# Optimization experiments

Hardware: AMD Instinct MI355X
Metric: run time of the kernel (lower is better)

## Reference

```python
import jax, jax.numpy as jnp
import numpy as np

N_NODES = 100000
N_EDGES = 1600000
IN_FEATS = 128
OUT_FEATS = 64


def setup_inputs() -> dict:
    key = jax.random.key(0)
    k1, k2, k3, k4 = jax.random.split(key, 4)
    feat = jax.random.normal(k1, (N_NODES, IN_FEATS), dtype=jnp.float32)
    W = jax.random.normal(k2, (IN_FEATS, OUT_FEATS), dtype=jnp.float32) * (1.0 / np.sqrt(IN_FEATS))
    src = jax.random.randint(k3, (N_EDGES,), 0, N_NODES, dtype=jnp.int64)
    dst = jax.random.randint(k4, (N_EDGES,), 0, N_NODES, dtype=jnp.int64)
    return {"feat": feat, "W": W, "src": src, "dst": dst}


def reference(feat, W, src, dst):
    # Linear projection (bias=False): homogeneous graph -> shared fc
    ft = feat @ W  # [N, out]

    # per-edge dot-product score: e_ij = <ft[src], ft[dst]>
    a = jnp.sum(ft[src] * ft[dst], axis=-1)  # [E]

    # edge softmax segmented by destination node (numerically stable)
    neg_inf = jnp.finfo(a.dtype).min
    m = jax.ops.segment_max(a, dst, num_segments=N_NODES)  # [N]
    m = jnp.where(m == neg_inf, 0.0, m)  # guard zero-in-degree nodes
    e = jnp.exp(a - m[dst])  # [E]
    s = jax.ops.segment_sum(e, dst, num_segments=N_NODES)  # [N]
    s = jnp.where(s == 0.0, 1.0, s)
    sa = e / s[dst]  # [E]

    # weighted scatter-sum aggregation: out[i] = sum_{j in N(i)} sa_ij * ft[j]
    rst = jax.ops.segment_sum(ft[src] * sa[:, None], dst, num_segments=N_NODES)
    return rst
```

## Files before the change

kernel.cpp:

```cpp
#include <hip/hip_runtime.h>
#include <hip/hip_fp16.h>
#include <math.h>

#define N_NODES 100000
#define N_EDGES 1600000
#define IN_F    128
#define OUT_F   64
#define K_BKT     196
#define BKT_SHIFT 9
#define BKT_NODES 512
#define BKT_CAP   10240
#define CHUNK     4096
#define PBLKS     ((N_EDGES + CHUNK - 1) / CHUNK)
#define LTILES    (N_NODES / 16)
#define LBLKS     ((LTILES + 3) / 4)

typedef _Float16 half8 __attribute__((ext_vector_type(8)));
typedef float    f32x4 __attribute__((ext_vector_type(4)));


__global__ __launch_bounds__(256) void prep_kernel(const float* __restrict__ W,
                                                   _Float16* __restrict__ WT,
                                                   int* __restrict__ bcursor) {
    int t = threadIdx.x;
    if (t < K_BKT) bcursor[t] = 0;
    int n = t & 63, kh = t >> 6;
    _Float16 tmp[32];
#pragma unroll
    for (int j = 0; j < 32; ++j)
        tmp[j] = (_Float16)W[(size_t)(kh * 32 + j) * OUT_F + n];
#pragma unroll
    for (int v = 0; v < 4; ++v)
        *(half8*)(WT + (size_t)n * IN_F + kh * 32 + v * 8) = *(half8*)&tmp[v * 8];
}

__global__ __launch_bounds__(256) void partition_linear_kernel(const int* __restrict__ src,
                                                               const int* __restrict__ dst,
                                                               int* __restrict__ bcursor,
                                                               unsigned* __restrict__ staging,
                                                               const float* __restrict__ feat,
                                                               const _Float16* __restrict__ WT,
                                                               __half* __restrict__ fth) {
    __shared__ int hist[256], lbase[256], gbase[256], sc[256];
    __shared__ unsigned sval[CHUNK];
    __shared__ int spos[CHUNK];
    int t = threadIdx.x;
    if (blockIdx.x < PBLKS) {
        hist[t] = 0;
        __syncthreads();
        int beg = blockIdx.x * CHUNK;
        int end = min(beg + CHUNK, N_EDGES);
        for (int i = beg + t; i < end; i += 256)
            atomicAdd(&hist[dst[i] >> BKT_SHIFT], 1);
        __syncthreads();
        int v = hist[t];
        sc[t] = v;
        __syncthreads();
        for (int off = 1; off < 256; off <<= 1) {
            int add = (t >= off) ? sc[t - off] : 0;
            __syncthreads();
            sc[t] += add;
            __syncthreads();
        }
        lbase[t] = sc[t] - v;
        if (t < K_BKT && v) gbase[t] = t * BKT_CAP + atomicAdd(&bcursor[t], v);
        hist[t] = 0;
        __syncthreads();
        for (int i = beg + t; i < end; i += 256) {
            int s = src[i], d = dst[i];
            int b = d >> BKT_SHIFT;
            int r = atomicAdd(&hist[b], 1);
            int lp = lbase[b] + r;
            sval[lp] = (unsigned)s | ((unsigned)(d & (BKT_NODES - 1)) << 17);
            spos[lp] = gbase[b] + r;
        }
        __syncthreads();
        int n = end - beg;
        for (int p = t; p < n; p += 256) staging[spos[p]] = sval[p];
        return;
    }
    int gwave = (blockIdx.x - PBLKS) * 4 + (t >> 6);
    if (gwave >= LTILES) return;
    int lane = t & 63;
    int m = lane & 15, kg = lane >> 4;
    int r0 = gwave * 16;

    half8 fb[4][4];
#pragma unroll
    for (int kb = 0; kb < 4; ++kb)
#pragma unroll
        for (int nb = 0; nb < 4; ++nb)
            fb[kb][nb] = *(const half8*)(WT + (size_t)(nb * 16 + m) * IN_F + kb * 32 + kg * 8);

    f32x4 acc[4];
#pragma unroll
    for (int nb = 0; nb < 4; ++nb) acc[nb] = (f32x4){0.f, 0.f, 0.f, 0.f};

#pragma unroll
    for (int kb = 0; kb < 4; ++kb) {
        const float4* ap = (const float4*)(feat + (size_t)(r0 + m) * IN_F + kb * 32 + kg * 8);
        float4 a0 = ap[0], a1 = ap[1];
        half8 fa = {(_Float16)a0.x, (_Float16)a0.y, (_Float16)a0.z, (_Float16)a0.w,
                    (_Float16)a1.x, (_Float16)a1.y, (_Float16)a1.z, (_Float16)a1.w};
#pragma unroll
        for (int nb = 0; nb < 4; ++nb)
            acc[nb] = __builtin_amdgcn_mfma_f32_16x16x32_f16(fa, fb[kb][nb], acc[nb], 0, 0, 0);
    }
#pragma unroll
    for (int nb = 0; nb < 4; ++nb)
#pragma unroll
        for (int i = 0; i < 4; ++i)
            fth[(size_t)(r0 + kg * 4 + i) * OUT_F + nb * 16 + m] = __float2half_rn(acc[nb][i]);
}

__global__ __launch_bounds__(256) void place_kernel(const unsigned* __restrict__ staging,
                                                    const int* __restrict__ bcursor,
                                                    int* __restrict__ row_beg,
                                                    int* __restrict__ row_end,
                                                    int* __restrict__ edge_src) {
    __shared__ int cnt[BKT_NODES], sc[256], lcur[BKT_NODES];
    int t = threadIdx.x;
    cnt[t] = 0; cnt[t + 256] = 0;
    __syncthreads();
    int base = blockIdx.x * BKT_CAP;
    int n = bcursor[blockIdx.x];
    for (int i = t; i < n; i += 256)
        atomicAdd(&cnt[staging[base + i] >> 17], 1);
    __syncthreads();
    int v0 = cnt[2 * t], v1 = cnt[2 * t + 1];
    int ts = v0 + v1;
    sc[t] = ts;
    __syncthreads();
    for (int off = 1; off < 256; off <<= 1) {
        int add = (t >= off) ? sc[t - off] : 0;
        __syncthreads();
        sc[t] += add;
        __syncthreads();
    }
    int excl = sc[t] - ts;
    int node0 = blockIdx.x * BKT_NODES;
    int b0 = base + excl, b1 = base + excl + v0;
    lcur[2 * t]     = b0;
    lcur[2 * t + 1] = b1;
    if (node0 + 2 * t < N_NODES)     { row_beg[node0 + 2 * t] = b0;     row_end[node0 + 2 * t] = b0 + v0; }
    if (node0 + 2 * t + 1 < N_NODES) { row_beg[node0 + 2 * t + 1] = b1; row_end[node0 + 2 * t + 1] = b1 + v1; }
    __syncthreads();
    for (int i = base + t; i < base + n; i += 256) {
        unsigned u = staging[i];
        int pos = atomicAdd(&lcur[u >> 17], 1);
        edge_src[pos] = (int)(u & 0x1FFFFu);
    }
}

__global__ __launch_bounds__(256) void fused_node_kernel(const __half* __restrict__ fth,
                                                         const int* __restrict__ row_beg,
                                                         const int* __restrict__ row_end,
                                                         const int* __restrict__ edge_src,
                                                         float* __restrict__ out) {
    const float LOG2E = 1.44269504088896340736f;
    int wave = (blockIdx.x * 256 + threadIdx.x) >> 6;
    int lane = threadIdx.x & 63;
    if (wave >= N_NODES) return;
    int q = lane >> 4, ql = lane & 15;

    int beg = row_beg[wave];
    int end = row_end[wave];

    float2 rd = *(const float2*)(fth + (size_t)wave * OUT_F + 4 * ql);
    __half2 d01 = *(__half2*)&rd.x, d23 = *(__half2*)&rd.y;
    float fd0 = __half2float(d01.x) * LOG2E, fd1 = __half2float(d01.y) * LOG2E;
    float fd2 = __half2float(d23.x) * LOG2E, fd3 = __half2float(d23.y) * LOG2E;

    float m = -1e30f, l = 0.f;
    float a0 = 0.f, a1 = 0.f, a2 = 0.f, a3 = 0.f;

    for (int i = beg; i < end; i += 16) {
        int e0 = i + q, e1 = e0 + 4, e2 = e0 + 8, e3 = e0 + 12;
        bool u0 = e0 < end, u1 = e1 < end, u2 = e2 < end, u3 = e3 < end;
        int s0 = edge_src[u0 ? e0 : beg];
        int s1 = edge_src[u1 ? e1 : beg];
        int s2 = edge_src[u2 ? e2 : beg];
        int s3 = edge_src[u3 ? e3 : beg];
        float2 r0 = *(const float2*)(fth + (size_t)s0 * OUT_F + 4 * ql);
        float2 r1 = *(const float2*)(fth + (size_t)s1 * OUT_F + 4 * ql);
        float2 r2 = *(const float2*)(fth + (size_t)s2 * OUT_F + 4 * ql);
        float2 r3 = *(const float2*)(fth + (size_t)s3 * OUT_F + 4 * ql);
        __half2 A01 = *(__half2*)&r0.x, A23 = *(__half2*)&r0.y;
        __half2 B01 = *(__half2*)&r1.x, B23 = *(__half2*)&r1.y;
        __half2 C01 = *(__half2*)&r2.x, C23 = *(__half2*)&r2.y;
        __half2 D01 = *(__half2*)&r3.x, D23 = *(__half2*)&r3.y;
        float vA0 = __half2float(A01.x), vA1 = __half2float(A01.y);
        float vA2 = __half2float(A23.x), vA3 = __half2float(A23.y);
        float vB0 = __half2float(B01.x), vB1 = __half2float(B01.y);
        float vB2 = __half2float(B23.x), vB3 = __half2float(B23.y);
        float vC0 = __half2float(C01.x), vC1 = __half2float(C01.y);
        float vC2 = __half2float(C23.x), vC3 = __half2float(C23.y);
        float vD0 = __half2float(D01.x), vD1 = __half2float(D01.y);
        float vD2 = __half2float(D23.x), vD3 = __half2float(D23.y);

        float p0 = vA0 * fd0 + vA1 * fd1 + vA2 * fd2 + vA3 * fd3;
        float p1 = vB0 * fd0 + vB1 * fd1 + vB2 * fd2 + vB3 * fd3;
        float p2 = vC0 * fd0 + vC1 * fd1 + vC2 * fd2 + vC3 * fd3;
        float p3 = vD0 * fd0 + vD1 * fd1 + vD2 * fd2 + vD3 * fd3;
#pragma unroll
        for (int dd = 1; dd < 16; dd <<= 1) {
            p0 += __shfl_xor(p0, dd);
            p1 += __shfl_xor(p1, dd);
            p2 += __shfl_xor(p2, dd);
            p3 += __shfl_xor(p3, dd);
        }
        if (!u0) p0 = -1e30f;
        if (!u1) p1 = -1e30f;
        if (!u2) p2 = -1e30f;
        if (!u3) p3 = -1e30f;
        float nm = fmaxf(fmaxf(fmaxf(p0, p1), fmaxf(p2, p3)), m);
        float alpha = exp2f(m - nm);
        float w0 = exp2f(p0 - nm), w1 = exp2f(p1 - nm);
        float w2 = exp2f(p2 - nm), w3 = exp2f(p3 - nm);
        l = l * alpha + ((w0 + w1) + (w2 + w3));
        a0 = a0 * alpha + (w0 * vA0 + w1 * vB0) + (w2 * vC0 + w3 * vD0);
        a1 = a1 * alpha + (w0 * vA1 + w1 * vB1) + (w2 * vC1 + w3 * vD1);
        a2 = a2 * alpha + (w0 * vA2 + w1 * vB2) + (w2 * vC2 + w3 * vD2);
        a3 = a3 * alpha + (w0 * vA3 + w1 * vB3) + (w2 * vC3 + w3 * vD3);
        m = nm;
    }

#pragma unroll
    for (int dd = 16; dd <= 32; dd <<= 1) {
        float m2 = __shfl_xor(m, dd), l2 = __shfl_xor(l, dd);
        float b0 = __shfl_xor(a0, dd), b1 = __shfl_xor(a1, dd);
        float b2 = __shfl_xor(a2, dd), b3 = __shfl_xor(a3, dd);
        float M = fmaxf(m, m2);
        float e1 = exp2f(m - M), e2 = exp2f(m2 - M);
        l = l * e1 + l2 * e2;
        a0 = a0 * e1 + b0 * e2;
        a1 = a1 * e1 + b1 * e2;
        a2 = a2 * e1 + b2 * e2;
        a3 = a3 * e1 + b3 * e2;
        m = M;
    }
    if (q == 0) {
        float inv = (l > 0.f) ? 1.f / l : 0.f;
        *(float4*)(out + (size_t)wave * OUT_F + 4 * ql) =
            make_float4(a0 * inv, a1 * inv, a2 * inv, a3 * inv);
    }
}

extern "C" void kernel_launch(void* const* d_in, const int* in_sizes, int n_in,
                              void* d_out, int out_size, void* d_ws, size_t ws_size,
                              hipStream_t stream) {
    const float* feat = (const float*)d_in[0];
    const float* W    = (const float*)d_in[1];
    const int*   src  = (const int*)d_in[2];
    const int*   dst  = (const int*)d_in[3];
    float* out = (float*)d_out;

    __half*   fth      = (__half*)d_ws;
    unsigned* staging  = (unsigned*)((int*)d_ws + (size_t)N_NODES * OUT_F / 2);
    int*      edge_src = (int*)(staging + (size_t)K_BKT * BKT_CAP);
    int*      bcursor  = edge_src + (size_t)K_BKT * BKT_CAP;
    int*      row_beg  = bcursor + K_BKT;
    int*      row_end  = row_beg + N_NODES;
    _Float16* WT       = (_Float16*)(row_end + N_NODES);

    prep_kernel<<<1, 256, 0, stream>>>(W, WT, bcursor);
    partition_linear_kernel<<<PBLKS + LBLKS, 256, 0, stream>>>(src, dst, bcursor, staging,
                                                               feat, WT, fth);
    place_kernel<<<K_BKT, 256, 0, stream>>>(staging, bcursor, row_beg, row_end, edge_src);
    fused_node_kernel<<<(N_NODES * 64) / 256, 256, 0, stream>>>(fth, row_beg, row_end, edge_src, out);
}
```

Baseline: 205.0 us.

## Regroup pipeline stages and use 1024-thread blocks for partition and place

The prep kernel is dropped. The bucket-cursor reset becomes a memset, and the W transpose moves into an extra block of the partition kernel. The linear projection moves out of the partition launch and now runs alongside the bucket place step in a combined kernel. Partition and place now use 1024-thread blocks. The goal is fewer launches, better balance of the linear GEMM against the lighter place work, and more parallelism per bucket, at the cost of lower occupancy and more idle threads during the scans.

```diff
diff --git a/kernel.cpp b/kernel.cpp
--- a/kernel.cpp
+++ b/kernel.cpp
@@ -13,73 +13,112 @@
 #define CHUNK     4096
 #define PBLKS     ((N_EDGES + CHUNK - 1) / CHUNK)
 #define LTILES    (N_NODES / 16)
-#define LBLKS     ((LTILES + 3) / 4)
+#define LIN_BLKS  ((LTILES + 15) / 16)
 
 typedef _Float16 half8 __attribute__((ext_vector_type(8)));
 typedef float    f32x4 __attribute__((ext_vector_type(4)));
 
 
-__global__ __launch_bounds__(256) void prep_kernel(const float* __restrict__ W,
-                                                   _Float16* __restrict__ WT,
-                                                   int* __restrict__ bcursor) {
-    int t = threadIdx.x;
-    if (t < K_BKT) bcursor[t] = 0;
-    int n = t & 63, kh = t >> 6;
-    _Float16 tmp[32];
-#pragma unroll
-    for (int j = 0; j < 32; ++j)
-        tmp[j] = (_Float16)W[(size_t)(kh * 32 + j) * OUT_F + n];
-#pragma unroll
-    for (int v = 0; v < 4; ++v)
-        *(half8*)(WT + (size_t)n * IN_F + kh * 32 + v * 8) = *(half8*)&tmp[v * 8];
-}
-
-__global__ __launch_bounds__(256) void partition_linear_kernel(const int* __restrict__ src,
-                                                               const int* __restrict__ dst,
-                                                               int* __restrict__ bcursor,
-                                                               unsigned* __restrict__ staging,
-                                                               const float* __restrict__ feat,
-                                                               const _Float16* __restrict__ WT,
-                                                               __half* __restrict__ fth) {
+__global__ __launch_bounds__(1024) void partition_kernel(const int* __restrict__ src,
+                                                         const int* __restrict__ dst,
+                                                         int* __restrict__ bcursor,
+                                                         unsigned* __restrict__ staging,
+                                                         const float* __restrict__ W,
+                                                         _Float16* __restrict__ WT) {
     __shared__ int hist[256], lbase[256], gbase[256], sc[256];
     __shared__ unsigned sval[CHUNK];
     __shared__ int spos[CHUNK];
     int t = threadIdx.x;
-    if (blockIdx.x < PBLKS) {
-        hist[t] = 0;
-        __syncthreads();
-        int beg = blockIdx.x * CHUNK;
-        int end = min(beg + CHUNK, N_EDGES);
-        for (int i = beg + t; i < end; i += 256)
-            atomicAdd(&hist[dst[i] >> BKT_SHIFT], 1);
-        __syncthreads();
+    if (blockIdx.x >= PBLKS) {
+        if (t < 256) {
+            int n = t & 63, kh = t >> 6;
+            _Float16 tmp[32];
+#pragma unroll
+            for (int j = 0; j < 32; ++j)
+                tmp[j] = (_Float16)W[(size_t)(kh * 32 + j) * OUT_F + n];
+#pragma unroll
+            for (int v = 0; v < 4; ++v)
+                *(half8*)(WT + (size_t)n * IN_F + kh * 32 + v * 8) = *(half8*)&tmp[v * 8];
+        }
+        return;
+    }
+    if (t < 256) hist[t] = 0;
+    __syncthreads();
+    int beg = blockIdx.x * CHUNK;
+    int end = min(beg + CHUNK, N_EDGES);
+    for (int i = beg + t; i < end; i += 1024)
+        atomicAdd(&hist[dst[i] >> BKT_SHIFT], 1);
+    __syncthreads();
+    if (t < 256) sc[t] = hist[t];
+    __syncthreads();
+    for (int off = 1; off < 256; off <<= 1) {
+        int add = (t >= off && t < 256) ? sc[t - off] : 0;
+        __syncthreads();
+        if (t < 256) sc[t] += add;
+        __syncthreads();
+    }
+    if (t < 256) {
         int v = hist[t];
-        sc[t] = v;
-        __syncthreads();
-        for (int off = 1; off < 256; off <<= 1) {
-            int add = (t >= off) ? sc[t - off] : 0;
-            __syncthreads();
-            sc[t] += add;
-            __syncthreads();
-        }
         lbase[t] = sc[t] - v;
         if (t < K_BKT && v) gbase[t] = t * BKT_CAP + atomicAdd(&bcursor[t], v);
         hist[t] = 0;
-        __syncthreads();
-        for (int i = beg + t; i < end; i += 256) {
-            int s = src[i], d = dst[i];
-            int b = d >> BKT_SHIFT;
-            int r = atomicAdd(&hist[b], 1);
-            int lp = lbase[b] + r;
-            sval[lp] = (unsigned)s | ((unsigned)(d & (BKT_NODES - 1)) << 17);
-            spos[lp] = gbase[b] + r;
-        }
-        __syncthreads();
-        int n = end - beg;
-        for (int p = t; p < n; p += 256) staging[spos[p]] = sval[p];
+    }
+    __syncthreads();
+    for (int i = beg + t; i < end; i += 1024) {
+        int s = src[i], d = dst[i];
+        int b = d >> BKT_SHIFT;
+        int r = atomicAdd(&hist[b], 1);
+        int lp = lbase[b] + r;
+        sval[lp] = (unsigned)s | ((unsigned)(d & (BKT_NODES - 1)) << 17);
+        spos[lp] = gbase[b] + r;
+    }
+    __syncthreads();
+    int n = end - beg;
+    for (int p = t; p < n; p += 1024) staging[spos[p]] = sval[p];
+}
+
+__global__ __launch_bounds__(1024) void place_linear_kernel(const unsigned* __restrict__ staging,
+                                                            const int* __restrict__ bcursor,
+                                                            int* __restrict__ row_beg,
+                                                            int* __restrict__ row_end,
+                                                            int* __restrict__ edge_src,
+                                                            const float* __restrict__ feat,
+                                                            const _Float16* __restrict__ WT,
+                                                            __half* __restrict__ fth) {
+    __shared__ int cnt[BKT_NODES], sc[BKT_NODES], lcur[BKT_NODES];
+    int t = threadIdx.x;
+    if (blockIdx.x < K_BKT) {
+        if (t < BKT_NODES) cnt[t] = 0;
+        __syncthreads();
+        int base = blockIdx.x * BKT_CAP;
+        int n = bcursor[blockIdx.x];
+        for (int i = t; i < n; i += 1024)
+            atomicAdd(&cnt[staging[base + i] >> 17], 1);
+        __syncthreads();
+        if (t < BKT_NODES) sc[t] = cnt[t];
+        __syncthreads();
+        for (int off = 1; off < BKT_NODES; off <<= 1) {
+            int add = (t >= off && t < BKT_NODES) ? sc[t - off] : 0;
+            __syncthreads();
+            if (t < BKT_NODES) sc[t] += add;
+            __syncthreads();
+        }
+        if (t < BKT_NODES) {
+            int v = cnt[t];
+            int b0 = base + sc[t] - v;
+            lcur[t] = b0;
+            int node = blockIdx.x * BKT_NODES + t;
+            if (node < N_NODES) { row_beg[node] = b0; row_end[node] = b0 + v; }
+        }
+        __syncthreads();
+        for (int i = base + t; i < base + n; i += 1024) {
+            unsigned u = staging[i];
+            int pos = atomicAdd(&lcur[u >> 17], 1);
+            edge_src[pos] = (int)(u & 0x1FFFFu);
+        }
         return;
     }
-    int gwave = (blockIdx.x - PBLKS) * 4 + (t >> 6);
+    int gwave = (blockIdx.x - K_BKT) * 16 + (t >> 6);
     if (gwave >= LTILES) return;
     int lane = t & 63;
     int m = lane & 15, kg = lane >> 4;
@@ -111,45 +150,6 @@
 #pragma unroll
         for (int i = 0; i < 4; ++i)
             fth[(size_t)(r0 + kg * 4 + i) * OUT_F + nb * 16 + m] = __float2half_rn(acc[nb][i]);
-}
-
-__global__ __launch_bounds__(256) void place_kernel(const unsigned* __restrict__ staging,
-                                                    const int* __restrict__ bcursor,
-                                                    int* __restrict__ row_beg,
-                                                    int* __restrict__ row_end,
-                                                    int* __restrict__ edge_src) {
-    __shared__ int cnt[BKT_NODES], sc[256], lcur[BKT_NODES];
-    int t = threadIdx.x;
-    cnt[t] = 0; cnt[t + 256] = 0;
-    __syncthreads();
-    int base = blockIdx.x * BKT_CAP;
-    int n = bcursor[blockIdx.x];
-    for (int i = t; i < n; i += 256)
-        atomicAdd(&cnt[staging[base + i] >> 17], 1);
-    __syncthreads();
-    int v0 = cnt[2 * t], v1 = cnt[2 * t + 1];
-    int ts = v0 + v1;
-    sc[t] = ts;
-    __syncthreads();
-    for (int off = 1; off < 256; off <<= 1) {
-        int add = (t >= off) ? sc[t - off] : 0;
-        __syncthreads();
-        sc[t] += add;
-        __syncthreads();
-    }
-    int excl = sc[t] - ts;
-    int node0 = blockIdx.x * BKT_NODES;
-    int b0 = base + excl, b1 = base + excl + v0;
-    lcur[2 * t]     = b0;
-    lcur[2 * t + 1] = b1;
-    if (node0 + 2 * t < N_NODES)     { row_beg[node0 + 2 * t] = b0;     row_end[node0 + 2 * t] = b0 + v0; }
-    if (node0 + 2 * t + 1 < N_NODES) { row_beg[node0 + 2 * t + 1] = b1; row_end[node0 + 2 * t + 1] = b1 + v1; }
-    __syncthreads();
-    for (int i = base + t; i < base + n; i += 256) {
-        unsigned u = staging[i];
-        int pos = atomicAdd(&lcur[u >> 17], 1);
-        edge_src[pos] = (int)(u & 0x1FFFFu);
-    }
 }
 
 __global__ __launch_bounds__(256) void fused_node_kernel(const __half* __restrict__ fth,
@@ -263,9 +263,9 @@
     int*      row_end  = row_beg + N_NODES;
     _Float16* WT       = (_Float16*)(row_end + N_NODES);
 
-    prep_kernel<<<1, 256, 0, stream>>>(W, WT, bcursor);
-    partition_linear_kernel<<<PBLKS + LBLKS, 256, 0, stream>>>(src, dst, bcursor, staging,
-                                                               feat, WT, fth);
-    place_kernel<<<K_BKT, 256, 0, stream>>>(staging, bcursor, row_beg, row_end, edge_src);
+    hipMemsetAsync(bcursor, 0, K_BKT * sizeof(int), stream);
+    partition_kernel<<<PBLKS + 1, 1024, 0, stream>>>(src, dst, bcursor, staging, W, WT);
+    place_linear_kernel<<<K_BKT + LIN_BLKS, 1024, 0, stream>>>(staging, bcursor, row_beg,
+                                                               row_end, edge_src, feat, WT, fth);
     fused_node_kernel<<<(N_NODES * 64) / 256, 256, 0, stream>>>(fth, row_beg, row_end, edge_src, out);
 }
```

Result: no change. 205.5 us (+0.2%).
